# Optimization experiments

Measured on AMD Instinct MI355X. Metric: run time of the kernel, lower is better.

## Reference

```python
import jax, jax.numpy as jnp
import numpy as np

EPS = 1e-5

def _bn2d(x, g, b, m, v):
    s = (1, -1, 1, 1)
    return (x - m.reshape(s)) * (g.reshape(s) * jax.lax.rsqrt(v.reshape(s) + EPS)) + b.reshape(s)

def _bn1d(x, g, b, m, v):
    return (x - m) * (g * jax.lax.rsqrt(v + EPS)) + b

def _conv3x3(x, w, b):
    y = jax.lax.conv_general_dilated(x, w, (1, 1), ((1, 1), (1, 1)),
                                     dimension_numbers=('NCHW', 'OIHW', 'NCHW'))
    return y + b.reshape(1, -1, 1, 1)

def setup_inputs() -> dict:
    key = jax.random.key(0)
    ks = iter(jax.random.split(key, 64))
    B = 512
    d = {}
    d['anchor'] = jax.random.normal(next(ks), (B, 1, 16, 8), jnp.float32)
    d['positive'] = jax.random.normal(next(ks), (B, 1, 16, 8), jnp.float32)
    d['negative'] = jax.random.normal(next(ks), (B, 1, 16, 8), jnp.float32)

    def bn_params(c):
        g = jax.random.normal(next(ks), (c,), jnp.float32) * 0.1 + 1.0
        b = jax.random.normal(next(ks), (c,), jnp.float32) * 0.1
        m = jax.random.normal(next(ks), (c,), jnp.float32) * 0.1
        v = jax.random.uniform(next(ks), (c,), jnp.float32, 0.5, 1.5)
        return g, b, m, v

    d['bn0_g'], d['bn0_b'], d['bn0_m'], d['bn0_v'] = bn_params(1)
    d['conv1_w'] = jax.random.normal(next(ks), (64, 1, 3, 3), jnp.float32) * 0.1
    d['conv1_b'] = jax.random.normal(next(ks), (64,), jnp.float32) * 0.1
    d['bn1_g'], d['bn1_b'], d['bn1_m'], d['bn1_v'] = bn_params(64)
    d['conv2_w'] = jax.random.normal(next(ks), (64, 64, 3, 3), jnp.float32) * 0.04
    d['conv2_b'] = jax.random.normal(next(ks), (64,), jnp.float32) * 0.1
    d['bn2_g'], d['bn2_b'], d['bn2_m'], d['bn2_v'] = bn_params(64)
    # locally-connected: kernel_size=1 -> per-position unshared channel mix (o,c,h,w)
    d['lc1_w'] = jax.random.normal(next(ks), (64, 64, 16, 8), jnp.float32) * 0.125
    d['bn3_g'], d['bn3_b'], d['bn3_m'], d['bn3_v'] = bn_params(64)
    d['lc2_w'] = jax.random.normal(next(ks), (64, 64, 16, 8), jnp.float32) * 0.125
    d['bn4_g'], d['bn4_b'], d['bn4_m'], d['bn4_v'] = bn_params(64)
    d['fc1_w'] = jax.random.normal(next(ks), (512, 8192), jnp.float32) * 0.01
    d['fc1_b'] = jax.random.normal(next(ks), (512,), jnp.float32) * 0.1
    d['bnf1_g'], d['bnf1_b'], d['bnf1_m'], d['bnf1_v'] = bn_params(512)
    d['fc2_w'] = jax.random.normal(next(ks), (512, 512), jnp.float32) * 0.04
    d['fc2_b'] = jax.random.normal(next(ks), (512,), jnp.float32) * 0.1
    d['bnf2_g'], d['bnf2_b'], d['bnf2_m'], d['bnf2_v'] = bn_params(512)
    d['fc3_w'] = jax.random.normal(next(ks), (128, 512), jnp.float32) * 0.04
    d['fc3_b'] = jax.random.normal(next(ks), (128,), jnp.float32) * 0.1
    d['bnf3_g'], d['bnf3_b'], d['bnf3_m'], d['bnf3_v'] = bn_params(128)
    d['out_w'] = jax.random.normal(next(ks), (128, 128), jnp.float32) * 0.09
    d['out_b'] = jax.random.normal(next(ks), (128,), jnp.float32) * 0.1
    return d

def _embedding(x, p):
    x = _bn2d(x, p['bn0_g'], p['bn0_b'], p['bn0_m'], p['bn0_v'])
    x = _conv3x3(x, p['conv1_w'], p['conv1_b'])
    x = jax.nn.relu(_bn2d(x, p['bn1_g'], p['bn1_b'], p['bn1_m'], p['bn1_v']))
    x = _conv3x3(x, p['conv2_w'], p['conv2_b'])
    x = jax.nn.relu(_bn2d(x, p['bn2_g'], p['bn2_b'], p['bn2_m'], p['bn2_v']))
    # locally connected (kernel 1): per-position channel mix, no huge unfold intermediate
    x = jnp.einsum('bchw,ochw->bohw', x, p['lc1_w'])
    x = jax.nn.relu(_bn2d(x, p['bn3_g'], p['bn3_b'], p['bn3_m'], p['bn3_v']))
    x = jnp.einsum('bchw,ochw->bohw', x, p['lc2_w'])
    x = jax.nn.relu(_bn2d(x, p['bn4_g'], p['bn4_b'], p['bn4_m'], p['bn4_v']))
    # dropout is identity in eval mode
    x = x.reshape(x.shape[0], -1)  # (B, 8192)
    x = x @ p['fc1_w'].T + p['fc1_b']
    x = jax.nn.relu(_bn1d(x, p['bnf1_g'], p['bnf1_b'], p['bnf1_m'], p['bnf1_v']))
    x = x @ p['fc2_w'].T + p['fc2_b']
    x = jax.nn.relu(_bn1d(x, p['bnf2_g'], p['bnf2_b'], p['bnf2_m'], p['bnf2_v']))
    x = x @ p['fc3_w'].T + p['fc3_b']
    x = jax.nn.relu(_bn1d(x, p['bnf3_g'], p['bnf3_b'], p['bnf3_m'], p['bnf3_v']))
    return x @ p['out_w'].T + p['out_b']

def reference(anchor, positive, negative,
              bn0_g, bn0_b, bn0_m, bn0_v,
              conv1_w, conv1_b, bn1_g, bn1_b, bn1_m, bn1_v,
              conv2_w, conv2_b, bn2_g, bn2_b, bn2_m, bn2_v,
              lc1_w, bn3_g, bn3_b, bn3_m, bn3_v,
              lc2_w, bn4_g, bn4_b, bn4_m, bn4_v,
              fc1_w, fc1_b, bnf1_g, bnf1_b, bnf1_m, bnf1_v,
              fc2_w, fc2_b, bnf2_g, bnf2_b, bnf2_m, bnf2_v,
              fc3_w, fc3_b, bnf3_g, bnf3_b, bnf3_m, bnf3_v,
              out_w, out_b):
    p = dict(bn0_g=bn0_g, bn0_b=bn0_b, bn0_m=bn0_m, bn0_v=bn0_v,
             conv1_w=conv1_w, conv1_b=conv1_b, bn1_g=bn1_g, bn1_b=bn1_b, bn1_m=bn1_m, bn1_v=bn1_v,
             conv2_w=conv2_w, conv2_b=conv2_b, bn2_g=bn2_g, bn2_b=bn2_b, bn2_m=bn2_m, bn2_v=bn2_v,
             lc1_w=lc1_w, bn3_g=bn3_g, bn3_b=bn3_b, bn3_m=bn3_m, bn3_v=bn3_v,
             lc2_w=lc2_w, bn4_g=bn4_g, bn4_b=bn4_b, bn4_m=bn4_m, bn4_v=bn4_v,
             fc1_w=fc1_w, fc1_b=fc1_b, bnf1_g=bnf1_g, bnf1_b=bnf1_b, bnf1_m=bnf1_m, bnf1_v=bnf1_v,
             fc2_w=fc2_w, fc2_b=fc2_b, bnf2_g=bnf2_g, bnf2_b=bnf2_b, bnf2_m=bnf2_m, bnf2_v=bnf2_v,
             fc3_w=fc3_w, fc3_b=fc3_b, bnf3_g=bnf3_g, bnf3_b=bnf3_b, bnf3_m=bnf3_m, bnf3_v=bnf3_v,
             out_w=out_w, out_b=out_b)
    return (_embedding(anchor, p), _embedding(positive, p), _embedding(negative, p))
```

## Files before the change

kernel.cpp:

```cpp
#include <hip/hip_runtime.h>
#include <math.h>

#define EPS 1e-5f
#define FD 8192

typedef __attribute__((ext_vector_type(8))) __bf16 bf16x8;
typedef __attribute__((ext_vector_type(4))) float f32x4;

static __device__ __forceinline__ f32x4 mfma16(bf16x8 a, bf16x8 b, f32x4 c) {
    return __builtin_amdgcn_mfma_f32_16x16x32_bf16(a, b, c, 0, 0, 0);
}

__global__ __launch_bounds__(256) void k_prep_frags(
    const float* __restrict__ w1, const float* __restrict__ w2,
    __bf16* __restrict__ w1frag, __bf16* __restrict__ w2frag) {
    const int bb = blockIdx.x, t = threadIdx.x;
    if (bb == 0) {
        const int lane = t & 63, w = t >> 6;
        const int q = lane >> 4, li = lane & 15;
        const int o = w * 16 + li;
        bf16x8 v;
#pragma unroll
        for (int j = 0; j < 8; ++j) {
            int k = q * 8 + j;
            v[j] = (k < 9) ? (__bf16)w1[o * 9 + k] : (__bf16)0.0f;
        }
        *(bf16x8*)(w1frag + t * 8) = v;
    } else {
        const int id = (bb - 1) * 256 + t;
        const int lane = id & 63;
        const int w = (id >> 6) & 3;
        const int chunk = (id >> 8) & 1;
        const int tap = id >> 9;
        const int q = lane >> 4, li = lane & 15;
        const int o = w * 16 + li;
        const int c0 = chunk * 32 + q * 8;
        bf16x8 v;
#pragma unroll
        for (int j = 0; j < 8; ++j)
            v[j] = (__bf16)w2[(o * 64 + c0 + j) * 9 + tap];
        *(bf16x8*)(w2frag + (size_t)id * 8) = v;
    }
}

__global__ __launch_bounds__(256) void k_conv_mega(
    const float* __restrict__ inA, const float* __restrict__ inP, const float* __restrict__ inN,
    const float* __restrict__ bn0g, const float* __restrict__ bn0b,
    const float* __restrict__ bn0m, const float* __restrict__ bn0v,
    const __bf16* __restrict__ w1frag, const float* __restrict__ b1,
    const float* __restrict__ bn1g, const float* __restrict__ bn1b,
    const float* __restrict__ bn1m, const float* __restrict__ bn1v,
    const __bf16* __restrict__ w2frag, const float* __restrict__ b2,
    const float* __restrict__ bn2g, const float* __restrict__ bn2b,
    const float* __restrict__ bn2m, const float* __restrict__ bn2v,
    __bf16* __restrict__ act,
    const float* __restrict__ lc1, const float* __restrict__ lc2,
    const float* __restrict__ fc1w, const float* __restrict__ fc2w,
    const float* __restrict__ fc3w, const float* __restrict__ outw,
    __bf16* __restrict__ lc1frag, __bf16* __restrict__ lc2frag,
    __bf16* __restrict__ fc1Wb, __bf16* __restrict__ wf23) {
    const int bb = blockIdx.x;
    const int t = threadIdx.x;
    __shared__ __align__(16) char smem[43136];

    if (bb >= 1536) {
        const int pb = bb - 1536;
        float (*wbuf)[130] = (float(*)[130])smem;
        if (pb < 128) {
            const int layer = pb >> 6, o = pb & 63;
            const int wo = o >> 4, lo = o & 15;
            const float* src = (layer ? lc2 : lc1) + (size_t)o * 8192;
            __bf16* dst = layer ? lc2frag : lc1frag;
#pragma unroll
            for (int pass = 0; pass < 8; ++pass) {
                int i = pass * 1024 + t * 4;
                float4 v = *(const float4*)(src + i);
                int c = i >> 7, p = i & 127;
                wbuf[c][p + 0] = v.x; wbuf[c][p + 1] = v.y;
                wbuf[c][p + 2] = v.z; wbuf[c][p + 3] = v.w;
            }
            __syncthreads();
#pragma unroll
            for (int pass = 0; pass < 4; ++pass) {
                int slot = pass * 256 + t;
                int p = slot >> 3, chunk = (slot >> 2) & 1, q = slot & 3;
                bf16x8 v;
#pragma unroll
                for (int j = 0; j < 8; ++j)
                    v[j] = (__bf16)wbuf[chunk * 32 + q * 8 + j][p];
                *(bf16x8*)(dst + ((size_t)((p * 2 + chunk) * 4 + wo) * 64 + q * 16 + lo) * 8) = v;
            }
        } else if (pb < 640) {
            const int n = pb - 128;
            const float* src = fc1w + (size_t)n * 8192;
            __bf16* dst = fc1Wb + (size_t)n * 8192;
#pragma unroll
            for (int pass = 0; pass < 8; ++pass) {
                int i = pass * 1024 + t * 4;
                float4 v = *(const float4*)(src + i);
                int c = i >> 7, p = i & 127;
                wbuf[c][p + 0] = v.x; wbuf[c][p + 1] = v.y;
                wbuf[c][p + 2] = v.z; wbuf[c][p + 3] = v.w;
            }
            __syncthreads();
#pragma unroll
            for (int pass = 0; pass < 16; ++pass) {
                int kA = (pass * 256 + t) * 2;
                int c = kA & 63, p = kA >> 6;
                __bf16 tmp[2];
                tmp[0] = (__bf16)wbuf[c][p];
                tmp[1] = (__bf16)wbuf[c + 1][p];
                *(unsigned int*)(dst + kA) = *(unsigned int*)tmp;
            }
        } else {
            int i = (pb - 640) * 256 + t;
            float v;
            if (i < 262144) v = fc2w[i];
            else if (i < 327680) v = fc3w[i - 262144];
            else v = outw[i - 327680];
            wf23[i] = (__bf16)v;
        }
        return;
    }

    const int b = bb;
    const int lane = t & 63, w = t >> 6;
    const int q = lane >> 4, li = lane & 15;
    const int n0 = w * 16;
    const int o = n0 + li;
    const float* src = (b < 512 ? inA : (b < 1024 ? inP : inN)) + (size_t)(b & 511) * 128;

    float* xpad = (float*)smem;
    __bf16* A1 = (__bf16*)(smem + 768);
    __bf16* Xp = (__bf16*)(smem + 11008);
    float* s1 = (float*)(smem + 42112);
    float* sh1 = (float*)(smem + 42368);
    float* s2 = (float*)(smem + 42624);
    float* sh2 = (float*)(smem + 42880);

    bf16x8 w1f = *(const bf16x8*)(w1frag + (size_t)(w * 64 + lane) * 8);
    bf16x8 w2f[18];
#pragma unroll
    for (int tap = 0; tap < 9; ++tap)
#pragma unroll
        for (int ch = 0; ch < 2; ++ch)
            w2f[tap * 2 + ch] = *(const bf16x8*)(w2frag +
                ((size_t)((tap * 2 + ch) * 4 + w) * 64 + lane) * 8);

    {
        int* xz = (int*)Xp;
        for (int i = t; i < 7776; i += 256) xz[i] = 0;
        if (t < 180) xpad[t] = 0.f;
        if (t < 64) {
            float sa = bn1g[t] * rsqrtf(bn1v[t] + EPS);
            s1[t] = sa;
            sh1[t] = (b1[t] - bn1m[t]) * sa + bn1b[t];
            float sb = bn2g[t] * rsqrtf(bn2v[t] + EPS);
            s2[t] = sb;
            sh2[t] = (b2[t] - bn2m[t]) * sb + bn2b[t];
        }
    }
    __syncthreads();
    if (t < 128) {
        float s0 = bn0g[0] * rsqrtf(bn0v[0] + EPS);
        float v = (src[t] - bn0m[0]) * s0 + bn0b[0];
        xpad[((t >> 3) + 1) * 10 + (t & 7) + 1] = v;
    }
    __syncthreads();
    {
        int p = t >> 1, half = t & 1;
        int r = p >> 3, cl = p & 7;
        bf16x8 v0, v1;
#pragma unroll
        for (int jj = 0; jj < 8; ++jj) {
            int j = half * 16 + jj;
            v0[jj] = (j < 9) ? (__bf16)xpad[(r + j / 3) * 10 + cl + (j % 3)] : (__bf16)0.f;
            int j2 = half * 16 + 8 + jj;
            v1[jj] = (j2 < 9) ? (__bf16)xpad[(r + j2 / 3) * 10 + cl + (j2 % 3)] : (__bf16)0.f;
        }
        *(bf16x8*)&A1[p * 40 + half * 16] = v0;
        *(bf16x8*)&A1[p * 40 + half * 16 + 8] = v1;
    }
    __syncthreads();
    {
        const float sco = s1[o], sho = sh1[o];
#pragma unroll
        for (int m = 0; m < 8; ++m) {
            bf16x8 a = *(const bf16x8*)&A1[(m * 16 + li) * 40 + q * 8];
            f32x4 z = {0.f, 0.f, 0.f, 0.f};
            f32x4 d = mfma16(a, w1f, z);
#pragma unroll
            for (int r = 0; r < 4; ++r) {
                int p = m * 16 + q * 4 + r;
                float v = fmaxf(d[r] * sco + sho, 0.f);
                Xp[(((p >> 3) + 1) * 12 + (p & 7) + 1) * 72 + o] = (__bf16)v;
            }
        }
    }
    __syncthreads();
    f32x4 accA[4], accB[4];
#pragma unroll
    for (int i = 0; i < 4; ++i) {
        accA[i] = (f32x4){0.f, 0.f, 0.f, 0.f};
        accB[i] = (f32x4){0.f, 0.f, 0.f, 0.f};
    }
    {
        const int cl = li & 7;
#pragma unroll
        for (int mp = 0; mp < 4; ++mp) {
            const int r0 = mp * 4 + (li >> 3);
            const int base0 = (r0 * 12 + cl) * 72 + q * 8;
            const int base1 = base0 + 1728;
#pragma unroll
            for (int tap = 0; tap < 9; ++tap) {
                const int tofs = ((tap / 3) * 12 + (tap % 3)) * 72;
#pragma unroll
                for (int ch = 0; ch < 2; ++ch) {
                    bf16x8 a0 = *(const bf16x8*)&Xp[base0 + tofs + ch * 32];
                    bf16x8 a1 = *(const bf16x8*)&Xp[base1 + tofs + ch * 32];
                    accA[mp] = mfma16(a0, w2f[tap * 2 + ch], accA[mp]);
                    accB[mp] = mfma16(a1, w2f[tap * 2 + ch], accB[mp]);
                }
            }
        }
    }
    __syncthreads();
    {
        const float sco = s2[o], sho = sh2[o];
#pragma unroll
        for (int mp = 0; mp < 4; ++mp) {
#pragma unroll
            for (int r = 0; r < 4; ++r) {
                int p0 = mp * 32 + q * 4 + r;
                Xp[p0 * 72 + o] = (__bf16)fmaxf(accA[mp][r] * sco + sho, 0.f);
                Xp[(p0 + 16) * 72 + o] = (__bf16)fmaxf(accB[mp][r] * sco + sho, 0.f);
            }
        }
    }
    __syncthreads();
    {
        int p = t >> 1, half = t & 1;
        const __bf16* rp = Xp + p * 72 + half * 32;
        __bf16* ob = act + (size_t)b * FD + p * 64 + half * 32;
        *(bf16x8*)ob = *(const bf16x8*)rp;
        *(bf16x8*)(ob + 8) = *(const bf16x8*)(rp + 8);
        *(bf16x8*)(ob + 16) = *(const bf16x8*)(rp + 16);
        *(bf16x8*)(ob + 24) = *(const bf16x8*)(rp + 24);
    }
}

__global__ __launch_bounds__(256) void k_lc_mfma(
    const __bf16* __restrict__ lc1frag, const __bf16* __restrict__ lc2frag,
    const float* __restrict__ bn3g, const float* __restrict__ bn3b,
    const float* __restrict__ bn3m, const float* __restrict__ bn3v,
    const float* __restrict__ bn4g, const float* __restrict__ bn4b,
    const float* __restrict__ bn4m, const float* __restrict__ bn4v,
    __bf16* __restrict__ act) {
    const int p = blockIdx.x;
    const int b0 = blockIdx.y * 128;
    const int t = threadIdx.x;
    const int lane = t & 63, w = t >> 6;
    const int q = lane >> 4, li = lane & 15;
    const int n0 = w * 16;

    __shared__ __align__(16) __bf16 xs[128 * 72];
    __shared__ __align__(16) __bf16 ys[128 * 72];
    __shared__ float s3[64], sh3[64], s4[64], sh4[64];

    if (t < 64) {
        float sa = bn3g[t] * rsqrtf(bn3v[t] + EPS);
        s3[t] = sa; sh3[t] = bn3b[t] - bn3m[t] * sa;
        float sb = bn4g[t] * rsqrtf(bn4v[t] + EPS);
        s4[t] = sb; sh4[t] = bn4b[t] - bn4m[t] * sb;
    }
    {
        int s = t >> 1, half = t & 1;
        const __bf16* rp = act + (size_t)(b0 + s) * FD + p * 64 + half * 32;
        __bf16* xp = xs + s * 72 + half * 32;
        *(bf16x8*)xp = *(const bf16x8*)rp;
        *(bf16x8*)(xp + 8) = *(const bf16x8*)(rp + 8);
        *(bf16x8*)(xp + 16) = *(const bf16x8*)(rp + 16);
        *(bf16x8*)(xp + 24) = *(const bf16x8*)(rp + 24);
    }
    bf16x8 w1a = *(const bf16x8*)(lc1frag + ((size_t)((p * 2 + 0) * 4 + w) * 64 + lane) * 8);
    bf16x8 w1b = *(const bf16x8*)(lc1frag + ((size_t)((p * 2 + 1) * 4 + w) * 64 + lane) * 8);
    bf16x8 w2a = *(const bf16x8*)(lc2frag + ((size_t)((p * 2 + 0) * 4 + w) * 64 + lane) * 8);
    bf16x8 w2b = *(const bf16x8*)(lc2frag + ((size_t)((p * 2 + 1) * 4 + w) * 64 + lane) * 8);
    __syncthreads();
    {
        const float sco = s3[n0 + li], sho = sh3[n0 + li];
#pragma unroll
        for (int m = 0; m < 8; ++m) {
            bf16x8 a0 = *(const bf16x8*)&xs[(m * 16 + li) * 72 + q * 8];
            bf16x8 a1 = *(const bf16x8*)&xs[(m * 16 + li) * 72 + 32 + q * 8];
            f32x4 acc = {0.f, 0.f, 0.f, 0.f};
            acc = mfma16(a0, w1a, acc);
            acc = mfma16(a1, w1b, acc);
#pragma unroll
            for (int r = 0; r < 4; ++r) {
                int bl = m * 16 + q * 4 + r;
                ys[bl * 72 + n0 + li] = (__bf16)fmaxf(acc[r] * sco + sho, 0.f);
            }
        }
    }
    __syncthreads();
    {
        const float sco = s4[n0 + li], sho = sh4[n0 + li];
#pragma unroll
        for (int m = 0; m < 8; ++m) {
            bf16x8 a0 = *(const bf16x8*)&ys[(m * 16 + li) * 72 + q * 8];
            bf16x8 a1 = *(const bf16x8*)&ys[(m * 16 + li) * 72 + 32 + q * 8];
            f32x4 acc = {0.f, 0.f, 0.f, 0.f};
            acc = mfma16(a0, w2a, acc);
            acc = mfma16(a1, w2b, acc);
#pragma unroll
            for (int r = 0; r < 4; ++r) {
                int bl = m * 16 + q * 4 + r;
                xs[bl * 72 + n0 + li] = (__bf16)fmaxf(acc[r] * sco + sho, 0.f);
            }
        }
    }
    __syncthreads();
    {
        int s = t >> 1, half = t & 1;
        const __bf16* rp = xs + s * 72 + half * 32;
        __bf16* ob = act + (size_t)(b0 + s) * FD + p * 64 + half * 32;
        *(bf16x8*)ob = *(const bf16x8*)rp;
        *(bf16x8*)(ob + 8) = *(const bf16x8*)(rp + 8);
        *(bf16x8*)(ob + 16) = *(const bf16x8*)(rp + 16);
        *(bf16x8*)(ob + 24) = *(const bf16x8*)(rp + 24);
    }
}

__global__ __launch_bounds__(256) void k_fc1_mfma(
    const __bf16* __restrict__ A, const __bf16* __restrict__ Wb,
    float* __restrict__ part) {
    const int t = threadIdx.x;
    const int lane = t & 63, w = t >> 6;
    const int q = lane >> 4, li = lane & 15;
    const int m0 = blockIdx.x * 128, n0 = blockIdx.y * 128;
    const int k0 = blockIdx.z * 1024;
    const int wm = (w & 1) * 64, wn = (w >> 1) * 64;

    __shared__ __align__(16) __bf16 As[128 * 72];
    __shared__ __align__(16) __bf16 Bs[128 * 72];

    f32x4 acc[4][4];
#pragma unroll
    for (int i = 0; i < 4; ++i)
#pragma unroll
        for (int j = 0; j < 4; ++j) acc[i][j] = (f32x4){0.f, 0.f, 0.f, 0.f};

    const int row = t >> 1, half = t & 1;
    const __bf16* Ag = A + (size_t)(m0 + row) * 8192 + k0 + half * 32;
    const __bf16* Bg = Wb + (size_t)(n0 + row) * 8192 + k0 + half * 32;

    bf16x8 pa0 = *(const bf16x8*)Ag, pa1 = *(const bf16x8*)(Ag + 8);
    bf16x8 pa2 = *(const bf16x8*)(Ag + 16), pa3 = *(const bf16x8*)(Ag + 24);
    bf16x8 pb0 = *(const bf16x8*)Bg, pb1 = *(const bf16x8*)(Bg + 8);
    bf16x8 pb2 = *(const bf16x8*)(Bg + 16), pb3 = *(const bf16x8*)(Bg + 24);

    for (int step = 0; step < 16; ++step) {
        __bf16* as = &As[row * 72 + half * 32];
        __bf16* bs = &Bs[row * 72 + half * 32];
        *(bf16x8*)as = pa0; *(bf16x8*)(as + 8) = pa1;
        *(bf16x8*)(as + 16) = pa2; *(bf16x8*)(as + 24) = pa3;
        *(bf16x8*)bs = pb0; *(bf16x8*)(bs + 8) = pb1;
        *(bf16x8*)(bs + 16) = pb2; *(bf16x8*)(bs + 24) = pb3;
        __syncthreads();
        Ag += 64; Bg += 64;
        if (step < 15) {
            pa0 = *(const bf16x8*)Ag; pa1 = *(const bf16x8*)(Ag + 8);
            pa2 = *(const bf16x8*)(Ag + 16); pa3 = *(const bf16x8*)(Ag + 24);
            pb0 = *(const bf16x8*)Bg; pb1 = *(const bf16x8*)(Bg + 8);
            pb2 = *(const bf16x8*)(Bg + 16); pb3 = *(const bf16x8*)(Bg + 24);
        }
#pragma unroll
        for (int kc = 0; kc < 2; ++kc) {
            bf16x8 af[4], bfr[4];
#pragma unroll
            for (int i = 0; i < 4; ++i)
                af[i] = *(const bf16x8*)&As[(wm + i * 16 + li) * 72 + kc * 32 + q * 8];
#pragma unroll
            for (int j = 0; j < 4; ++j)
                bfr[j] = *(const bf16x8*)&Bs[(wn + j * 16 + li) * 72 + kc * 32 + q * 8];
#pragma unroll
            for (int i = 0; i < 4; ++i)
#pragma unroll
                for (int j = 0; j < 4; ++j)
                    acc[i][j] = mfma16(af[i], bfr[j], acc[i][j]);
        }
        __syncthreads();
    }
    float* pp = part + (size_t)blockIdx.z * 786432;
#pragma unroll
    for (int i = 0; i < 4; ++i) {
#pragma unroll
        for (int r = 0; r < 4; ++r) {
            int m = m0 + wm + i * 16 + q * 4 + r;
#pragma unroll
            for (int j = 0; j < 4; ++j) {
                int n = n0 + wn + j * 16 + li;
                pp[(size_t)m * 512 + n] = acc[i][j][r];
            }
        }
    }
}

__global__ __launch_bounds__(256) void k_fc2_cr(
    const float* __restrict__ part,
    const float* __restrict__ b1f,
    const float* __restrict__ g1, const float* __restrict__ bb1,
    const float* __restrict__ m1, const float* __restrict__ v1,
    const __bf16* __restrict__ W2, const float* __restrict__ b2f,
    const float* __restrict__ g2, const float* __restrict__ bb2,
    const float* __restrict__ m2, const float* __restrict__ v2,
    __bf16* __restrict__ out) {
    const int t = threadIdx.x;
    const int lane = t & 63, w = t >> 6;
    const int q = lane >> 4, li = lane & 15;
    const int m0 = blockIdx.x * 32;

    __shared__ __align__(16) __bf16 Ared[32 * 520];
    __shared__ float esc[512], ehh[512];

    for (int n = t; n < 512; n += 256) {
        float s = g1[n] * rsqrtf(v1[n] + EPS);
        esc[n] = s;
        ehh[n] = (b1f[n] - m1[n]) * s + bb1[n];
    }
    __syncthreads();
    {
        const int row = t >> 3, seg = t & 7;
#pragma unroll
        for (int j = 0; j < 16; ++j) {
            int k4 = seg * 16 + j;
            size_t off = (size_t)(m0 + row) * 512 + k4 * 4;
            float vx = 0.f, vy = 0.f, vz = 0.f, vw = 0.f;
#pragma unroll
            for (int z = 0; z < 8; ++z) {
                float4 s = *(const float4*)(part + (size_t)z * 786432 + off);
                vx += s.x; vy += s.y; vz += s.z; vw += s.w;
            }
            float vv[4] = {vx, vy, vz, vw};
            __bf16 o4[4];
#pragma unroll
            for (int jj = 0; jj < 4; ++jj) {
                int k = k4 * 4 + jj;
                o4[jj] = (__bf16)fmaxf(vv[jj] * esc[k] + ehh[k], 0.f);
            }
            *(uint2*)&Ared[row * 520 + k4 * 4] = *(uint2*)o4;
        }
    }
    __syncthreads();
    f32x4 acc[2][8];
#pragma unroll
    for (int i = 0; i < 2; ++i)
#pragma unroll
        for (int j = 0; j < 8; ++j) acc[i][j] = (f32x4){0.f, 0.f, 0.f, 0.f};
    for (int k0 = 0; k0 < 512; k0 += 32) {
        bf16x8 af[2];
#pragma unroll
        for (int i = 0; i < 2; ++i)
            af[i] = *(const bf16x8*)&Ared[(i * 16 + li) * 520 + k0 + q * 8];
#pragma unroll
        for (int j = 0; j < 8; ++j) {
            int n = w * 128 + j * 16 + li;
            bf16x8 bf = *(const bf16x8*)(W2 + (size_t)n * 512 + k0 + q * 8);
#pragma unroll
            for (int i = 0; i < 2; ++i)
                acc[i][j] = mfma16(af[i], bf, acc[i][j]);
        }
    }
#pragma unroll
    for (int j = 0; j < 8; ++j) {
        int n = w * 128 + j * 16 + li;
        float sc = g2[n] * rsqrtf(v2[n] + EPS);
        float hh = (b2f[n] - m2[n]) * sc + bb2[n];
#pragma unroll
        for (int i = 0; i < 2; ++i)
#pragma unroll
            for (int r = 0; r < 4; ++r) {
                int m = m0 + i * 16 + q * 4 + r;
                float x = acc[i][j][r] * sc + hh;
                out[(size_t)m * 512 + n] = (__bf16)fmaxf(x, 0.f);
            }
    }
}

__global__ __launch_bounds__(256) void k_fc3out(
    const __bf16* __restrict__ A, const __bf16* __restrict__ W3,
    const __bf16* __restrict__ Wo,
    const float* __restrict__ b3,
    const float* __restrict__ bng, const float* __restrict__ bnb,
    const float* __restrict__ bnm, const float* __restrict__ bnv,
    const float* __restrict__ bo, float* __restrict__ out) {
    const int t = threadIdx.x;
    const int lane = t & 63, w = t >> 6;
    const int q = lane >> 4, li = lane & 15;
    const int m0 = blockIdx.x * 32;
    const int wn = w * 32;

    __shared__ __align__(16) __bf16 y3[32 * 136];

    f32x4 acc[2][2];
#pragma unroll
    for (int i = 0; i < 2; ++i)
#pragma unroll
        for (int j = 0; j < 2; ++j) acc[i][j] = (f32x4){0.f, 0.f, 0.f, 0.f};
    for (int k0 = 0; k0 < 512; k0 += 32) {
        bf16x8 af[2], bfr[2];
#pragma unroll
        for (int i = 0; i < 2; ++i)
            af[i] = *(const bf16x8*)(A + (size_t)(m0 + i * 16 + li) * 512 + k0 + q * 8);
#pragma unroll
        for (int j = 0; j < 2; ++j) {
            int n = wn + j * 16 + li;
            bfr[j] = *(const bf16x8*)(W3 + (size_t)n * 512 + k0 + q * 8);
        }
#pragma unroll
        for (int i = 0; i < 2; ++i)
#pragma unroll
            for (int j = 0; j < 2; ++j)
                acc[i][j] = mfma16(af[i], bfr[j], acc[i][j]);
    }
#pragma unroll
    for (int j = 0; j < 2; ++j) {
        int n = wn + j * 16 + li;
        float sc = bng[n] * rsqrtf(bnv[n] + EPS);
        float hh = bnb[n] - bnm[n] * sc;
        float bi = b3[n];
#pragma unroll
        for (int i = 0; i < 2; ++i)
#pragma unroll
            for (int r = 0; r < 4; ++r) {
                int m = i * 16 + q * 4 + r;
                float x = (acc[i][j][r] + bi) * sc + hh;
                y3[m * 136 + n] = (__bf16)fmaxf(x, 0.f);
            }
    }
    __syncthreads();
    f32x4 acc2[2][2];
#pragma unroll
    for (int i = 0; i < 2; ++i)
#pragma unroll
        for (int j = 0; j < 2; ++j) acc2[i][j] = (f32x4){0.f, 0.f, 0.f, 0.f};
#pragma unroll
    for (int step = 0; step < 4; ++step) {
        const int k0 = step * 32;
        bf16x8 af[2], bfr[2];
#pragma unroll
        for (int i = 0; i < 2; ++i)
            af[i] = *(const bf16x8*)&y3[(i * 16 + li) * 136 + k0 + q * 8];
#pragma unroll
        for (int j = 0; j < 2; ++j) {
            int n = wn + j * 16 + li;
            bfr[j] = *(const bf16x8*)(Wo + (size_t)n * 128 + k0 + q * 8);
        }
#pragma unroll
        for (int i = 0; i < 2; ++i)
#pragma unroll
            for (int j = 0; j < 2; ++j)
                acc2[i][j] = mfma16(af[i], bfr[j], acc2[i][j]);
    }
#pragma unroll
    for (int j = 0; j < 2; ++j) {
        int n = wn + j * 16 + li;
        float bi = bo[n];
#pragma unroll
        for (int i = 0; i < 2; ++i)
#pragma unroll
            for (int r = 0; r < 4; ++r) {
                int m = m0 + i * 16 + q * 4 + r;
                out[(size_t)m * 128 + n] = acc2[i][j][r] + bi;
            }
    }
}

extern "C" void kernel_launch(void* const* d_in, const int* in_sizes, int n_in,
                              void* d_out, int out_size, void* d_ws, size_t ws_size,
                              hipStream_t stream) {
    const float* inA    = (const float*)d_in[0];
    const float* inP    = (const float*)d_in[1];
    const float* inN    = (const float*)d_in[2];
    const float* bn0g   = (const float*)d_in[3];
    const float* bn0b   = (const float*)d_in[4];
    const float* bn0m   = (const float*)d_in[5];
    const float* bn0v   = (const float*)d_in[6];
    const float* conv1w = (const float*)d_in[7];
    const float* conv1b = (const float*)d_in[8];
    const float* bn1g   = (const float*)d_in[9];
    const float* bn1b   = (const float*)d_in[10];
    const float* bn1m   = (const float*)d_in[11];
    const float* bn1v   = (const float*)d_in[12];
    const float* conv2w = (const float*)d_in[13];
    const float* conv2b = (const float*)d_in[14];
    const float* bn2g   = (const float*)d_in[15];
    const float* bn2b   = (const float*)d_in[16];
    const float* bn2m   = (const float*)d_in[17];
    const float* bn2v   = (const float*)d_in[18];
    const float* lc1w   = (const float*)d_in[19];
    const float* bn3g   = (const float*)d_in[20];
    const float* bn3b   = (const float*)d_in[21];
    const float* bn3m   = (const float*)d_in[22];
    const float* bn3v   = (const float*)d_in[23];
    const float* lc2w   = (const float*)d_in[24];
    const float* bn4g   = (const float*)d_in[25];
    const float* bn4b   = (const float*)d_in[26];
    const float* bn4m   = (const float*)d_in[27];
    const float* bn4v   = (const float*)d_in[28];
    const float* fc1w   = (const float*)d_in[29];
    const float* fc1b   = (const float*)d_in[30];
    const float* bnf1g  = (const float*)d_in[31];
    const float* bnf1b  = (const float*)d_in[32];
    const float* bnf1m  = (const float*)d_in[33];
    const float* bnf1v  = (const float*)d_in[34];
    const float* fc2w   = (const float*)d_in[35];
    const float* fc2b   = (const float*)d_in[36];
    const float* bnf2g  = (const float*)d_in[37];
    const float* bnf2b  = (const float*)d_in[38];
    const float* bnf2m  = (const float*)d_in[39];
    const float* bnf2v  = (const float*)d_in[40];
    const float* fc3w   = (const float*)d_in[41];
    const float* fc3b   = (const float*)d_in[42];
    const float* bnf3g  = (const float*)d_in[43];
    const float* bnf3b  = (const float*)d_in[44];
    const float* bnf3m  = (const float*)d_in[45];
    const float* bnf3v  = (const float*)d_in[46];
    const float* outw   = (const float*)d_in[47];
    const float* outb   = (const float*)d_in[48];

    char* wsb = (char*)d_ws;
    __bf16* w1frag  = (__bf16*)wsb;
    __bf16* w2frag  = w1frag + 2048;
    __bf16* lc1frag = w2frag + 36864;
    __bf16* lc2frag = lc1frag + 524288;
    __bf16* fc1Wb   = lc2frag + 524288;
    __bf16* wf23    = fc1Wb + 4194304;
    __bf16* act     = wf23 + 344064;
    __bf16* act4    = act + 12582912;
    float*  part    = (float*)(((uintptr_t)(act4 + 786432) + 15) & ~(uintptr_t)15);
    __bf16* wf2 = wf23;
    __bf16* wf3 = wf23 + 262144;
    __bf16* wfo = wf23 + 327680;

    k_prep_frags<<<19, 256, 0, stream>>>(conv1w, conv2w, w1frag, w2frag);

    k_conv_mega<<<3520, 256, 0, stream>>>(inA, inP, inN,
        bn0g, bn0b, bn0m, bn0v, w1frag, conv1b, bn1g, bn1b, bn1m, bn1v,
        w2frag, conv2b, bn2g, bn2b, bn2m, bn2v, act,
        lc1w, lc2w, fc1w, fc2w, fc3w, outw,
        lc1frag, lc2frag, fc1Wb, wf23);

    k_lc_mfma<<<dim3(128, 12), 256, 0, stream>>>(lc1frag, lc2frag,
        bn3g, bn3b, bn3m, bn3v, bn4g, bn4b, bn4m, bn4v, act);

    k_fc1_mfma<<<dim3(12, 4, 8), 256, 0, stream>>>(act, fc1Wb, part);

    k_fc2_cr<<<48, 256, 0, stream>>>(part,
        fc1b, bnf1g, bnf1b, bnf1m, bnf1v,
        wf2, fc2b, bnf2g, bnf2b, bnf2m, bnf2v, act4);

    k_fc3out<<<48, 256, 0, stream>>>(act4, wf3, wfo, fc3b,
        bnf3g, bnf3b, bnf3m, bnf3v, outb, (float*)d_out);
}
```

Measured before the change: 287.6 us.

## Halve fc1 split-K factor and tile fc2 over N for more blocks

fc1 now splits K into 4 chunks of 2048 instead of 8 of 1024, which halves the partial-sum traffic that fc2 must read and reduce. fc2 is re-tiled into a 24x8 grid of 64x64 output tiles instead of 48 blocks each computing full 512-wide rows, so many more blocks share the work. The trade-off is that each fc2 block now recomputes the split-K reduction and BN1 for its 64 rows, repeated across the 8 N-blocks, and fc1 runs only 192 blocks with longer K loops. The BN2 epilogue is rewritten algebraically but is equivalent.

```diff
diff --git a/kernel.cpp b/kernel.cpp
--- a/kernel.cpp
+++ b/kernel.cpp
@@ -339,7 +339,7 @@
     const int lane = t & 63, w = t >> 6;
     const int q = lane >> 4, li = lane & 15;
     const int m0 = blockIdx.x * 128, n0 = blockIdx.y * 128;
-    const int k0 = blockIdx.z * 1024;
+    const int k0 = blockIdx.z * 2048;
     const int wm = (w & 1) * 64, wn = (w >> 1) * 64;
 
     __shared__ __align__(16) __bf16 As[128 * 72];
@@ -360,7 +360,7 @@
     bf16x8 pb0 = *(const bf16x8*)Bg, pb1 = *(const bf16x8*)(Bg + 8);
     bf16x8 pb2 = *(const bf16x8*)(Bg + 16), pb3 = *(const bf16x8*)(Bg + 24);
 
-    for (int step = 0; step < 16; ++step) {
+    for (int step = 0; step < 32; ++step) {
         __bf16* as = &As[row * 72 + half * 32];
         __bf16* bs = &Bs[row * 72 + half * 32];
         *(bf16x8*)as = pa0; *(bf16x8*)(as + 8) = pa1;
@@ -369,7 +369,7 @@
         *(bf16x8*)(bs + 16) = pb2; *(bf16x8*)(bs + 24) = pb3;
         __syncthreads();
         Ag += 64; Bg += 64;
-        if (step < 15) {
+        if (step < 31) {
             pa0 = *(const bf16x8*)Ag; pa1 = *(const bf16x8*)(Ag + 8);
             pa2 = *(const bf16x8*)(Ag + 16); pa3 = *(const bf16x8*)(Ag + 24);
             pb0 = *(const bf16x8*)Bg; pb1 = *(const bf16x8*)(Bg + 8);
@@ -407,7 +407,7 @@
     }
 }
 
-__global__ __launch_bounds__(256) void k_fc2_cr(
+__global__ __launch_bounds__(256) void k_fc2_mfma(
     const float* __restrict__ part,
     const float* __restrict__ b1f,
     const float* __restrict__ g1, const float* __restrict__ bb1,
@@ -419,9 +419,10 @@
     const int t = threadIdx.x;
     const int lane = t & 63, w = t >> 6;
     const int q = lane >> 4, li = lane & 15;
-    const int m0 = blockIdx.x * 32;
-
-    __shared__ __align__(16) __bf16 Ared[32 * 520];
+    const int m0 = blockIdx.x * 64, n0 = blockIdx.y * 64;
+    const int wm = (w & 1) * 32, wn = (w >> 1) * 32;
+
+    __shared__ __align__(16) __bf16 Ared[64 * 520];
     __shared__ float esc[512], ehh[512];
 
     for (int n = t; n < 512; n += 256) {
@@ -431,60 +432,68 @@
     }
     __syncthreads();
     {
-        const int row = t >> 3, seg = t & 7;
-#pragma unroll
-        for (int j = 0; j < 16; ++j) {
-            int k4 = seg * 16 + j;
+        const int row = t >> 2, seg = t & 3;
+#pragma unroll
+        for (int j = 0; j < 32; ++j) {
+            int k4 = seg + j * 4;
             size_t off = (size_t)(m0 + row) * 512 + k4 * 4;
-            float vx = 0.f, vy = 0.f, vz = 0.f, vw = 0.f;
-#pragma unroll
-            for (int z = 0; z < 8; ++z) {
-                float4 s = *(const float4*)(part + (size_t)z * 786432 + off);
-                vx += s.x; vy += s.y; vz += s.z; vw += s.w;
-            }
-            float vv[4] = {vx, vy, vz, vw};
+            float4 s0 = *(const float4*)(part + off);
+            float4 s1 = *(const float4*)(part + 786432 + off);
+            float4 s2 = *(const float4*)(part + 2 * 786432 + off);
+            float4 s3 = *(const float4*)(part + 3 * 786432 + off);
+            float v[4] = {s0.x + s1.x + s2.x + s3.x, s0.y + s1.y + s2.y + s3.y,
+                          s0.z + s1.z + s2.z + s3.z, s0.w + s1.w + s2.w + s3.w};
             __bf16 o4[4];
 #pragma unroll
             for (int jj = 0; jj < 4; ++jj) {
                 int k = k4 * 4 + jj;
-                o4[jj] = (__bf16)fmaxf(vv[jj] * esc[k] + ehh[k], 0.f);
+                o4[jj] = (__bf16)fmaxf(v[jj] * esc[k] + ehh[k], 0.f);
             }
             *(uint2*)&Ared[row * 520 + k4 * 4] = *(uint2*)o4;
         }
     }
     __syncthreads();
-    f32x4 acc[2][8];
+    f32x4 acc[2][2];
 #pragma unroll
     for (int i = 0; i < 2; ++i)
 #pragma unroll
-        for (int j = 0; j < 8; ++j) acc[i][j] = (f32x4){0.f, 0.f, 0.f, 0.f};
+        for (int j = 0; j < 2; ++j) acc[i][j] = (f32x4){0.f, 0.f, 0.f, 0.f};
     for (int k0 = 0; k0 < 512; k0 += 32) {
-        bf16x8 af[2];
-#pragma unroll
-        for (int i = 0; i < 2; ++i)
-            af[i] = *(const bf16x8*)&Ared[(i * 16 + li) * 520 + k0 + q * 8];
-#pragma unroll
-        for (int j = 0; j < 8; ++j) {
-            int n = w * 128 + j * 16 + li;
-            bf16x8 bf = *(const bf16x8*)(W2 + (size_t)n * 512 + k0 + q * 8);
-#pragma unroll
-            for (int i = 0; i < 2; ++i)
-                acc[i][j] = mfma16(af[i], bf, acc[i][j]);
-        }
-    }
-#pragma unroll
-    for (int j = 0; j < 8; ++j) {
-        int n = w * 128 + j * 16 + li;
-        float sc = g2[n] * rsqrtf(v2[n] + EPS);
-        float hh = (b2f[n] - m2[n]) * sc + bb2[n];
-#pragma unroll
-        for (int i = 0; i < 2; ++i)
-#pragma unroll
-            for (int r = 0; r < 4; ++r) {
-                int m = m0 + i * 16 + q * 4 + r;
-                float x = acc[i][j][r] * sc + hh;
+        bf16x8 af[2], bfr[2];
+#pragma unroll
+        for (int j = 0; j < 2; ++j) {
+            int n = n0 + wn + j * 16 + li;
+            bfr[j] = *(const bf16x8*)(W2 + (size_t)n * 512 + k0 + q * 8);
+        }
+#pragma unroll
+        for (int i = 0; i < 2; ++i)
+            af[i] = *(const bf16x8*)&Ared[(wm + i * 16 + li) * 520 + k0 + q * 8];
+#pragma unroll
+        for (int i = 0; i < 2; ++i)
+#pragma unroll
+            for (int j = 0; j < 2; ++j)
+                acc[i][j] = mfma16(af[i], bfr[j], acc[i][j]);
+    }
+    float bi[2], sc[2], hh[2];
+#pragma unroll
+    for (int j = 0; j < 2; ++j) {
+        int n = n0 + wn + j * 16 + li;
+        bi[j] = b2f[n];
+        sc[j] = g2[n] * rsqrtf(v2[n] + EPS);
+        hh[j] = bb2[n] - m2[n] * sc[j];
+    }
+#pragma unroll
+    for (int i = 0; i < 2; ++i) {
+#pragma unroll
+        for (int r = 0; r < 4; ++r) {
+            int m = m0 + wm + i * 16 + q * 4 + r;
+#pragma unroll
+            for (int j = 0; j < 2; ++j) {
+                int n = n0 + wn + j * 16 + li;
+                float x = (acc[i][j][r] + bi[j]) * sc[j] + hh[j];
                 out[(size_t)m * 512 + n] = (__bf16)fmaxf(x, 0.f);
             }
+        }
     }
 }
 
@@ -655,9 +664,9 @@
     k_lc_mfma<<<dim3(128, 12), 256, 0, stream>>>(lc1frag, lc2frag,
         bn3g, bn3b, bn3m, bn3v, bn4g, bn4b, bn4m, bn4v, act);
 
-    k_fc1_mfma<<<dim3(12, 4, 8), 256, 0, stream>>>(act, fc1Wb, part);
-
-    k_fc2_cr<<<48, 256, 0, stream>>>(part,
+    k_fc1_mfma<<<dim3(12, 4, 4), 256, 0, stream>>>(act, fc1Wb, part);
+
+    k_fc2_mfma<<<dim3(24, 8), 256, 0, stream>>>(part,
         fc1b, bnf1g, bnf1b, bnf1m, bnf1v,
         wf2, fc2b, bnf2g, bnf2b, bnf2m, bnf2v, act4);
 
```

New measurement: 273.8 us. -4.8%, faster.
